# Kernel tuning notes

Hardware: AMD Instinct MI355X
Metric: run time of the kernel (lower is better)

## Reference

```python
import jax, jax.numpy as jnp
import numpy as np

B, GH, GW, DIM, NH = 1, 48, 64, 1536, 16
HD = DIM // NH          # 96
C = HD // 2             # 48, divisible by 3 as the rope split requires
L = max(GH, GW)


def setup_inputs() -> dict:
    key = jax.random.key(0)
    ks = jax.random.split(key, 6)
    x = jax.random.normal(ks[0], (B, GH * GW, DIM), jnp.float32)
    w_init = lambda k: jax.random.normal(k, (DIM, DIM), jnp.float32) * 0.02
    # rope frequency table: theta[p, j] = p / 10000^(j/C); freqs = exp(i*theta)
    pos = jnp.arange(L, dtype=jnp.float32)[:, None]
    inv = 10000.0 ** (-jnp.arange(C, dtype=jnp.float32) / C)
    theta = pos * inv[None, :]
    return {
        "x": x,
        "wq": w_init(ks[1]), "bq": jnp.zeros((DIM,), jnp.float32),
        "wk": w_init(ks[2]), "bk": jnp.zeros((DIM,), jnp.float32),
        "wv": w_init(ks[3]), "bv": jnp.zeros((DIM,), jnp.float32),
        "wo": w_init(ks[4]), "bo": jnp.zeros((DIM,), jnp.float32),
        "freqs_cos": jnp.cos(theta), "freqs_sin": jnp.sin(theta),
        "h": GH, "w": GW,
    }


def rope_apply_spatial(x, freqs_cos, freqs_sin, h, w):
    # x: [b, s, n, d] with s == h*w. Complex rotation done in real arithmetic.
    b, s, n, d = x.shape
    c = d // 2
    c3 = c // 3
    # channel groups: [0:c3] identity (ones), [c3:2c3] rotated by h-position,
    # [2c3:3c3] rotated by w-position  (matches freqs.split + cat in torch)
    cos_hw = jnp.concatenate([
        jnp.ones((h, w, c3), x.dtype),
        jnp.broadcast_to(freqs_cos[:h, None, c3:2 * c3], (h, w, c3)),
        jnp.broadcast_to(freqs_cos[None, :w, 2 * c3:3 * c3], (h, w, c3)),
    ], axis=-1).reshape(1, s, 1, c)
    sin_hw = jnp.concatenate([
        jnp.zeros((h, w, c3), x.dtype),
        jnp.broadcast_to(freqs_sin[:h, None, c3:2 * c3], (h, w, c3)),
        jnp.broadcast_to(freqs_sin[None, :w, 2 * c3:3 * c3], (h, w, c3)),
    ], axis=-1).reshape(1, s, 1, c)
    xc = x.reshape(b, s, n, c, 2)
    xr, xi = xc[..., 0], xc[..., 1]
    yr = xr * cos_hw - xi * sin_hw
    yi = xr * sin_hw + xi * cos_hw
    return jnp.stack([yr, yi], axis=-1).reshape(b, s, n, d)


def reference(x, wq, bq, wk, bk, wv, bv, wo, bo, freqs_cos, freqs_sin, h, w):
    b, s, _ = x.shape
    q = (x @ wq + bq).reshape(b, s, NH, HD)
    k = (x @ wk + bk).reshape(b, s, NH, HD)
    v = (x @ wv + bv).reshape(b, s, NH, HD)
    q = rope_apply_spatial(q, freqs_cos, freqs_sin, h, w)
    k = rope_apply_spatial(k, freqs_cos, freqs_sin, h, w)
    scale = 1.0 / jnp.sqrt(jnp.asarray(HD, q.dtype))
    scores = jnp.einsum('bqnd,bknd->bnqk', q, k) * scale  # [b, n, s, s]
    attn = jax.nn.softmax(scores, axis=-1)
    out = jnp.einsum('bnqk,bknd->bqnd', attn, v).reshape(b, s, NH * HD)
    return out @ wo + bo
```

## Files before the change

### kernel.cpp

```cpp
#include <hip/hip_runtime.h>
#include <math.h>

#define S_LEN 3072
#define DIM 1536
#define NHEADS 16
#define HDIM 96
#define NPAIR 48

typedef __attribute__((ext_vector_type(8))) _Float16 half8;
typedef __attribute__((ext_vector_type(4))) _Float16 half4v;
typedef __attribute__((ext_vector_type(2))) _Float16 half2v;
typedef __attribute__((ext_vector_type(4))) float f32x4;

__device__ inline void gload16(const void* g, void* l) {
    __builtin_amdgcn_global_load_lds(
        (const __attribute__((address_space(1))) void*)g,
        (__attribute__((address_space(3))) void*)l, 16, 0, 0);
}

__global__ __launch_bounds__(256)
void convert_f32_f16(const float* __restrict__ src, _Float16* __restrict__ dst, int n4)
{
    int i = blockIdx.x * 256 + threadIdx.x;
    if (i < n4) {
        float4 v = *(const float4*)&src[(size_t)i * 4];
        half4v h = { (_Float16)v.x, (_Float16)v.y, (_Float16)v.z, (_Float16)v.w };
        *(half4v*)&dst[(size_t)i * 4] = h;
    }
}

__global__ __launch_bounds__(256)
void transpose_w(const float* __restrict__ w0, const float* __restrict__ w1,
                 const float* __restrict__ w2, const float* __restrict__ w3,
                 _Float16* __restrict__ wt)
{
    __shared__ _Float16 t[64][68];
    const int z = blockIdx.z;
    const float* W = (z == 0) ? w0 : (z == 1) ? w1 : (z == 2) ? w2 : w3;
    _Float16* O = wt + (size_t)z * DIM * DIM;
    const int k0 = blockIdx.y * 64, n0 = blockIdx.x * 64;
    const int tid = threadIdx.x;
    const int r = tid >> 4, c4 = (tid & 15) * 4;
#pragma unroll
    for (int g = 0; g < 4; g++) {
        int kk = r + g * 16;
        float4 v = *(const float4*)&W[(size_t)(k0 + kk) * DIM + n0 + c4];
        t[c4 + 0][kk] = (_Float16)v.x; t[c4 + 1][kk] = (_Float16)v.y;
        t[c4 + 2][kk] = (_Float16)v.z; t[c4 + 3][kk] = (_Float16)v.w;
    }
    __syncthreads();
    const int nr = tid >> 2, ks = (tid & 3) * 16;
#pragma unroll
    for (int s = 0; s < 4; s++)
        *(ushort4*)&O[(size_t)(n0 + nr) * DIM + k0 + ks + s * 4] =
            *(ushort4*)&t[nr][ks + s * 4];
}

template<bool QKV>
__global__ __launch_bounds__(256)
void gemm_f16(const _Float16* __restrict__ X,
              const _Float16* __restrict__ W0t, const _Float16* __restrict__ W1t,
              const _Float16* __restrict__ W2t,
              const float* __restrict__ B0, const float* __restrict__ B1,
              const float* __restrict__ B2,
              const float* __restrict__ fc, const float* __restrict__ fs,
              void* __restrict__ outv)
{
    __shared__ __align__(16) _Float16 As[128][64];
    __shared__ __align__(16) _Float16 Bs[128][64];

    const int tid = threadIdx.x;
    const int w = tid >> 6, lane = tid & 63;
    const int ln = lane & 15, quad = lane >> 4;
    const int bz = blockIdx.z;
    const _Float16* Wt = W0t; const float* bias = B0;
    if (QKV) { if (bz == 1) { Wt = W1t; bias = B1; } else if (bz == 2) { Wt = W2t; bias = B2; } }
    const int m0 = blockIdx.y * 128, n0 = blockIdx.x * 128;
    const int wm = w >> 1, wn = w & 1;
    const int row8 = lane >> 3, cch = lane & 7;
    const int gch = cch ^ row8;

    f32x4 acc[4][4];
#pragma unroll
    for (int i = 0; i < 4; i++)
#pragma unroll
        for (int j = 0; j < 4; j++) acc[i][j] = (f32x4){0.f, 0.f, 0.f, 0.f};

    for (int k0 = 0; k0 < DIM; k0 += 64) {
        __syncthreads();
#pragma unroll
        for (int j = 0; j < 4; j++) {
            const int r = w * 32 + j * 8;
            gload16(X  + (size_t)(m0 + r + row8) * DIM + k0 + gch * 8, &As[r][0]);
            gload16(Wt + (size_t)(n0 + r + row8) * DIM + k0 + gch * 8, &Bs[r][0]);
        }
        __syncthreads();

        half8 a[4][2], b[4][2];
#pragma unroll
        for (int mt = 0; mt < 4; mt++) {
            int m = wm * 64 + mt * 16 + ln;
#pragma unroll
            for (int ks = 0; ks < 2; ks++) {
                int s = (ks * 4 + quad) ^ (ln & 7);
                a[mt][ks] = *(const half8*)&As[m][s * 8];
            }
        }
#pragma unroll
        for (int nt = 0; nt < 4; nt++) {
            int n = wn * 64 + nt * 16 + ln;
#pragma unroll
            for (int ks = 0; ks < 2; ks++) {
                int s = (ks * 4 + quad) ^ (ln & 7);
                b[nt][ks] = *(const half8*)&Bs[n][s * 8];
            }
        }
#pragma unroll
        for (int ks = 0; ks < 2; ks++)
#pragma unroll
            for (int mt = 0; mt < 4; mt++)
#pragma unroll
                for (int nt = 0; nt < 4; nt++)
                    acc[mt][nt] = __builtin_amdgcn_mfma_f32_16x16x32_f16(
                        a[mt][ks], b[nt][ks], acc[mt][nt], 0, 0, 0);
    }

#pragma unroll
    for (int nt = 0; nt < 4; nt++) {
        int col = n0 + wn * 64 + nt * 16 + ln;
        float bv = bias[col];
        int head = col / HDIM, hd = col % HDIM;
        int jc = hd >> 1;
        bool isreal = (ln & 1) == 0;
#pragma unroll
        for (int mt = 0; mt < 4; mt++) {
            int row0 = m0 + wm * 64 + mt * 16 + quad * 4;
            if (QKV && bz == 2) {
                half4v p;
#pragma unroll
                for (int r = 0; r < 4; r++) p[r] = (_Float16)(acc[mt][nt][r] + bv);
                *(half4v*)&((_Float16*)outv)[(((size_t)2 * NHEADS + head) * HDIM + hd) * S_LEN + row0] = p;
            } else if (QKV) {
                float v[4], vp[4];
#pragma unroll
                for (int r = 0; r < 4; r++) v[r] = acc[mt][nt][r] + bv;
#pragma unroll
                for (int r = 0; r < 4; r++) vp[r] = __shfl_xor(v[r], 1);
#pragma unroll
                for (int r = 0; r < 4; r++) {
                    int srow = row0 + r;
                    int pos = (jc < 32) ? (srow >> 6) : (srow & 63);
                    float c  = fc[pos * NPAIR + jc];
                    float sn = fs[pos * NPAIR + jc];
                    float xr = isreal ? v[r] : vp[r];
                    float xi = isreal ? vp[r] : v[r];
                    float rot = isreal ? (xr * c - xi * sn) : (xr * sn + xi * c);
                    float outval = (jc < 16) ? v[r] : rot;
                    ((_Float16*)outv)[(((size_t)bz * NHEADS + head) * S_LEN + srow) * HDIM + hd]
                        = (_Float16)outval;
                }
            } else {
#pragma unroll
                for (int r = 0; r < 4; r++)
                    ((float*)outv)[(size_t)(row0 + r) * DIM + col] = acc[mt][nt][r] + bv;
            }
        }
    }
}

__global__ __launch_bounds__(256, 3)
void attn_mfma_kernel(const _Float16* __restrict__ qh, const _Float16* __restrict__ kh,
                      const _Float16* __restrict__ vtg, _Float16* __restrict__ aoh)
{
    __shared__ __align__(16) _Float16 Ks[2][64][104];
    __shared__ __align__(16) _Float16 Vt[2][96][72];

    const int tid  = threadIdx.x;
    const int wid  = tid >> 6;
    const int p    = wid >> 1;
    const int wp   = wid & 1;
    const int lane = tid & 63;
    const int ln   = lane & 15;
    const int quad = lane >> 4;
    const int h    = blockIdx.y;
    const int q0   = blockIdx.x * 64;
    const float scale_ = 0.10206207261596577f * 1.4426950408889634f;
    const int NT = (S_LEN / 2) / 64;

    half8 aq[2][3];
#pragma unroll
    for (int qs = 0; qs < 2; qs++) {
        const _Float16* qrow = qh + (((size_t)h * S_LEN) + q0 + (wp * 2 + qs) * 16 + ln) * HDIM;
#pragma unroll
        for (int kb = 0; kb < 3; kb++) {
            half8 a = *(const half8*)&qrow[kb * 32 + quad * 8];
            half8 v;
#pragma unroll
            for (int i = 0; i < 8; i++) v[i] = (_Float16)((float)a[i] * scale_);
            aq[qs][kb] = v;
        }
    }

    f32x4 o[2][6];
#pragma unroll
    for (int qs = 0; qs < 2; qs++)
#pragma unroll
        for (int dn = 0; dn < 6; dn++) o[qs][dn] = (f32x4){0.f, 0.f, 0.f, 0.f};
    float m_[2] = {-INFINITY, -INFINITY}, l_[2] = {0.f, 0.f};

    const _Float16* kbase = kh + ((size_t)h * S_LEN + p * (S_LEN / 2)) * HDIM;
    const _Float16* vbase = vtg + (size_t)h * HDIM * S_LEN + p * (S_LEN / 2);

    const int tp = tid & 127;
    const int krow = tp >> 1, kc0 = (tp & 1) * 6;
    const _Float16* ksrc0 = kbase + (size_t)krow * HDIM + kc0 * 8;
    _Float16* kdst = &Ks[p][krow][kc0 * 8];
    const int vd0 = tp >> 3, vc = tp & 7;
    const _Float16* vsrc0 = vbase + (size_t)vd0 * S_LEN + vc * 8;
    _Float16* vdst = &Vt[p][vd0][(vc ^ (vd0 & 7)) * 8];

    uint4 kp0, kp1, kp2, kp3, kp4, kp5, vp0, vp1, vp2, vp3, vp4, vp5;
    kp0 = *(const uint4*)(ksrc0 + 0 * 8);  kp1 = *(const uint4*)(ksrc0 + 1 * 8);
    kp2 = *(const uint4*)(ksrc0 + 2 * 8);  kp3 = *(const uint4*)(ksrc0 + 3 * 8);
    kp4 = *(const uint4*)(ksrc0 + 4 * 8);  kp5 = *(const uint4*)(ksrc0 + 5 * 8);
    vp0 = *(const uint4*)(vsrc0 + 0 * 16 * S_LEN);
    vp1 = *(const uint4*)(vsrc0 + 1 * 16 * S_LEN);
    vp2 = *(const uint4*)(vsrc0 + 2 * 16 * S_LEN);
    vp3 = *(const uint4*)(vsrc0 + 3 * 16 * S_LEN);
    vp4 = *(const uint4*)(vsrc0 + 4 * 16 * S_LEN);
    vp5 = *(const uint4*)(vsrc0 + 5 * 16 * S_LEN);

    for (int kt = 0; kt < NT; ++kt) {
        __syncthreads();
        *(uint4*)(kdst + 0 * 8) = kp0;  *(uint4*)(kdst + 1 * 8) = kp1;
        *(uint4*)(kdst + 2 * 8) = kp2;  *(uint4*)(kdst + 3 * 8) = kp3;
        *(uint4*)(kdst + 4 * 8) = kp4;  *(uint4*)(kdst + 5 * 8) = kp5;
        *(uint4*)(vdst + 0 * 16 * 72) = vp0;  *(uint4*)(vdst + 1 * 16 * 72) = vp1;
        *(uint4*)(vdst + 2 * 16 * 72) = vp2;  *(uint4*)(vdst + 3 * 16 * 72) = vp3;
        *(uint4*)(vdst + 4 * 16 * 72) = vp4;  *(uint4*)(vdst + 5 * 16 * 72) = vp5;
        __syncthreads();

        if (kt + 1 < NT) {
            const _Float16* ks2 = ksrc0 + (size_t)(kt + 1) * 64 * HDIM;
            kp0 = *(const uint4*)(ks2 + 0 * 8);  kp1 = *(const uint4*)(ks2 + 1 * 8);
            kp2 = *(const uint4*)(ks2 + 2 * 8);  kp3 = *(const uint4*)(ks2 + 3 * 8);
            kp4 = *(const uint4*)(ks2 + 4 * 8);  kp5 = *(const uint4*)(ks2 + 5 * 8);
            __builtin_amdgcn_sched_barrier(0);
        }

        f32x4 s[2][4];
#pragma unroll
        for (int nb = 0; nb < 4; nb++) {
            half8 ak0 = *(const half8*)&Ks[p][nb * 16 + ln][0 * 32 + quad * 8];
            half8 ak1 = *(const half8*)&Ks[p][nb * 16 + ln][1 * 32 + quad * 8];
            half8 ak2 = *(const half8*)&Ks[p][nb * 16 + ln][2 * 32 + quad * 8];
#pragma unroll
            for (int qs = 0; qs < 2; qs++) {
                f32x4 acc = (f32x4){0.f, 0.f, 0.f, 0.f};
                acc = __builtin_amdgcn_mfma_f32_16x16x32_f16(ak0, aq[qs][0], acc, 0, 0, 0);
                acc = __builtin_amdgcn_mfma_f32_16x16x32_f16(ak1, aq[qs][1], acc, 0, 0, 0);
                acc = __builtin_amdgcn_mfma_f32_16x16x32_f16(ak2, aq[qs][2], acc, 0, 0, 0);
                s[qs][nb] = acc;
            }
        }

        half4v ap[2][4];
#pragma unroll
        for (int qs = 0; qs < 2; qs++) {
            float ma = fmaxf(fmaxf(s[qs][0][0], s[qs][0][1]), fmaxf(s[qs][0][2], s[qs][0][3]));
            float mb = fmaxf(fmaxf(s[qs][1][0], s[qs][1][1]), fmaxf(s[qs][1][2], s[qs][1][3]));
            float mc = fmaxf(fmaxf(s[qs][2][0], s[qs][2][1]), fmaxf(s[qs][2][2], s[qs][2][3]));
            float md = fmaxf(fmaxf(s[qs][3][0], s[qs][3][1]), fmaxf(s[qs][3][2], s[qs][3][3]));
            float mx = fmaxf(fmaxf(ma, mb), fmaxf(mc, md));
            if (!__all(mx <= m_[qs] + 8.0f)) {
                mx = fmaxf(mx, __shfl_xor(mx, 16));
                mx = fmaxf(mx, __shfl_xor(mx, 32));
                float mn = fmaxf(m_[qs], mx);
                float al = __builtin_amdgcn_exp2f(m_[qs] - mn);
                m_[qs] = mn;
                l_[qs] *= al;
#pragma unroll
                for (int dn = 0; dn < 6; dn++)
#pragma unroll
                    for (int r = 0; r < 4; r++) o[qs][dn][r] *= al;
            }
            float rs = 0.f;
            float mq = m_[qs];
#pragma unroll
            for (int nb = 0; nb < 4; nb++) {
                float p0 = __builtin_amdgcn_exp2f(s[qs][nb][0] - mq);
                float p1 = __builtin_amdgcn_exp2f(s[qs][nb][1] - mq);
                float p2 = __builtin_amdgcn_exp2f(s[qs][nb][2] - mq);
                float p3 = __builtin_amdgcn_exp2f(s[qs][nb][3] - mq);
                rs += (p0 + p1) + (p2 + p3);
                half4v pk = { (_Float16)p0, (_Float16)p1, (_Float16)p2, (_Float16)p3 };
                ap[qs][nb] = pk;
            }
            l_[qs] += rs;
        }

        if (kt + 1 < NT) {
            const _Float16* vs2 = vsrc0 + (kt + 1) * 64;
            vp0 = *(const uint4*)(vs2 + 0 * 16 * S_LEN);
            vp1 = *(const uint4*)(vs2 + 1 * 16 * S_LEN);
            vp2 = *(const uint4*)(vs2 + 2 * 16 * S_LEN);
            vp3 = *(const uint4*)(vs2 + 3 * 16 * S_LEN);
            vp4 = *(const uint4*)(vs2 + 4 * 16 * S_LEN);
            vp5 = *(const uint4*)(vs2 + 5 * 16 * S_LEN);
            __builtin_amdgcn_sched_barrier(0);
        }

#pragma unroll
        for (int nb = 0; nb < 4; nb++) {
            const int off = (((nb * 2 + (quad >> 1)) ^ (ln & 7)) * 8) + (quad & 1) * 4;
#pragma unroll
            for (int dn = 0; dn < 6; dn++) {
                half4v av = *(const half4v*)&Vt[p][dn * 16 + ln][off];
                o[0][dn] = __builtin_amdgcn_mfma_f32_16x16x16f16(av, ap[0][nb], o[0][dn], 0, 0, 0);
                o[1][dn] = __builtin_amdgcn_mfma_f32_16x16x16f16(av, ap[1][nb], o[1][dn], 0, 0, 0);
            }
        }
    }

    __syncthreads();
    float lt[2];
#pragma unroll
    for (int qs = 0; qs < 2; qs++) {
        float l = l_[qs];
        l += __shfl_xor(l, 16);
        l += __shfl_xor(l, 32);
        lt[qs] = l;
    }
    float*  scr = (float*)&Ks[0][0][0];
    float2* mlb = (float2*)&Vt[0][0][0];
    if (p == 1) {
#pragma unroll
        for (int qs = 0; qs < 2; qs++) {
            int row = (wp * 2 + qs) * 16 + ln;
            if (quad == 0) mlb[row] = make_float2(m_[qs], lt[qs]);
#pragma unroll
            for (int dn = 0; dn < 6; dn++)
                *(f32x4*)&scr[row * 100 + dn * 16 + quad * 4] = o[qs][dn];
        }
    }
    __syncthreads();
    if (p == 0) {
#pragma unroll
        for (int qs = 0; qs < 2; qs++) {
            int row = (wp * 2 + qs) * 16 + ln;
            float2 ml1 = mlb[row];
            float mm = fmaxf(m_[qs], ml1.x);
            float a0 = __builtin_amdgcn_exp2f(m_[qs] - mm);
            float a1 = __builtin_amdgcn_exp2f(ml1.x - mm);
            float li = 1.0f / (lt[qs] * a0 + ml1.y * a1);
            const size_t rowbase = (size_t)(q0 + row) * DIM + h * HDIM;
#pragma unroll
            for (int dn = 0; dn < 6; dn++) {
                f32x4 o1 = *(const f32x4*)&scr[row * 100 + dn * 16 + quad * 4];
                half4v pk;
#pragma unroll
                for (int r = 0; r < 4; r++)
                    pk[r] = (_Float16)((o[qs][dn][r] * a0 + o1[r] * a1) * li);
                *(half4v*)&aoh[rowbase + dn * 16 + quad * 4] = pk;
            }
        }
    }
}

extern "C" void kernel_launch(void* const* d_in, const int* in_sizes, int n_in,
                              void* d_out, int out_size, void* d_ws, size_t ws_size,
                              hipStream_t stream) {
    const float* x  = (const float*)d_in[0];
    const float* wq = (const float*)d_in[1];
    const float* bq = (const float*)d_in[2];
    const float* wk = (const float*)d_in[3];
    const float* bk = (const float*)d_in[4];
    const float* wv = (const float*)d_in[5];
    const float* bv = (const float*)d_in[6];
    const float* wo = (const float*)d_in[7];
    const float* bo = (const float*)d_in[8];
    const float* fc = (const float*)d_in[9];
    const float* fs = (const float*)d_in[10];
    float* out = (float*)d_out;

    const size_t per  = (size_t)NHEADS * S_LEN * HDIM;
    const size_t dim2 = (size_t)DIM * DIM;
    _Float16* hws  = (_Float16*)d_ws;
    _Float16* qkvh = hws;
    _Float16* qh   = qkvh;
    _Float16* kh   = qkvh + per;
    _Float16* vth  = qkvh + 2 * per;
    _Float16* xh   = hws + 3 * per;
    _Float16* wth  = hws + 4 * per;

    convert_f32_f16<<<(int)((S_LEN * DIM / 4 + 255) / 256), 256, 0, stream>>>(
        x, xh, S_LEN * DIM / 4);
    transpose_w<<<dim3(DIM / 64, DIM / 64, 4), 256, 0, stream>>>(wq, wk, wv, wo, wth);

    gemm_f16<true><<<dim3(DIM / 128, S_LEN / 128, 3), 256, 0, stream>>>(
        xh, wth, wth + dim2, wth + 2 * dim2, bq, bk, bv, fc, fs, qkvh);
    attn_mfma_kernel<<<dim3(S_LEN / 64, NHEADS), 256, 0, stream>>>(qh, kh, vth, xh);
    gemm_f16<false><<<dim3(DIM / 128, S_LEN / 128, 1), 256, 0, stream>>>(
        xh, wth + 3 * dim2, nullptr, nullptr, bo, nullptr, nullptr, fc, fs, out);
}
```

Measured before the change: 331.1 us.

## Double-buffer K via direct global-to-LDS loads; read V straight from global

```diff
diff --git a/kernel.cpp b/kernel.cpp
--- a/kernel.cpp
+++ b/kernel.cpp
@@ -172,8 +172,7 @@
 void attn_mfma_kernel(const _Float16* __restrict__ qh, const _Float16* __restrict__ kh,
                       const _Float16* __restrict__ vtg, _Float16* __restrict__ aoh)
 {
-    __shared__ __align__(16) _Float16 Ks[2][64][104];
-    __shared__ __align__(16) _Float16 Vt[2][96][72];
+    __shared__ __align__(16) _Float16 Kb[2][2][64 * 96];
 
     const int tid  = threadIdx.x;
     const int wid  = tid >> 6;
@@ -208,52 +207,53 @@
         for (int dn = 0; dn < 6; dn++) o[qs][dn] = (f32x4){0.f, 0.f, 0.f, 0.f};
     float m_[2] = {-INFINITY, -INFINITY}, l_[2] = {0.f, 0.f};
 
-    const _Float16* kbase = kh + ((size_t)h * S_LEN + p * (S_LEN / 2)) * HDIM;
-    const _Float16* vbase = vtg + (size_t)h * HDIM * S_LEN + p * (S_LEN / 2);
-
-    const int tp = tid & 127;
-    const int krow = tp >> 1, kc0 = (tp & 1) * 6;
-    const _Float16* ksrc0 = kbase + (size_t)krow * HDIM + kc0 * 8;
-    _Float16* kdst = &Ks[p][krow][kc0 * 8];
-    const int vd0 = tp >> 3, vc = tp & 7;
-    const _Float16* vsrc0 = vbase + (size_t)vd0 * S_LEN + vc * 8;
-    _Float16* vdst = &Vt[p][vd0][(vc ^ (vd0 & 7)) * 8];
-
-    uint4 kp0, kp1, kp2, kp3, kp4, kp5, vp0, vp1, vp2, vp3, vp4, vp5;
-    kp0 = *(const uint4*)(ksrc0 + 0 * 8);  kp1 = *(const uint4*)(ksrc0 + 1 * 8);
-    kp2 = *(const uint4*)(ksrc0 + 2 * 8);  kp3 = *(const uint4*)(ksrc0 + 3 * 8);
-    kp4 = *(const uint4*)(ksrc0 + 4 * 8);  kp5 = *(const uint4*)(ksrc0 + 5 * 8);
-    vp0 = *(const uint4*)(vsrc0 + 0 * 16 * S_LEN);
-    vp1 = *(const uint4*)(vsrc0 + 1 * 16 * S_LEN);
-    vp2 = *(const uint4*)(vsrc0 + 2 * 16 * S_LEN);
-    vp3 = *(const uint4*)(vsrc0 + 3 * 16 * S_LEN);
-    vp4 = *(const uint4*)(vsrc0 + 4 * 16 * S_LEN);
-    vp5 = *(const uint4*)(vsrc0 + 5 * 16 * S_LEN);
+    const char* kbase = (const char*)(kh + ((size_t)h * S_LEN + p * (S_LEN / 2)) * HDIM);
+
+    int koffb[6];
+#pragma unroll
+    for (int i = 0; i < 6; i++) {
+        int pc = i * 128 + (tid & 127);
+        int r  = pc / 12, c = pc - r * 12;
+        int rm = r % 12;
+        int cl = c - rm; if (cl < 0) cl += 12;
+        koffb[i] = r * 192 + cl * 16;
+    }
+    const int A0 = (quad + ln) % 12;
+    int ksel[3];
+    ksel[0] = A0 * 16;
+    { int t1 = A0 + 4; if (t1 >= 12) t1 -= 12; ksel[1] = t1 * 16; }
+    { int t2 = A0 + 8; if (t2 >= 12) t2 -= 12; ksel[2] = t2 * 16; }
+
+    const _Float16* vrow[6];
+#pragma unroll
+    for (int dn = 0; dn < 6; dn++)
+        vrow[dn] = vtg + (size_t)h * HDIM * S_LEN + (size_t)(dn * 16 + ln) * S_LEN
+                 + p * (S_LEN / 2) + quad * 4;
+
+#pragma unroll
+    for (int i = 0; i < 6; i++)
+        gload16(kbase + koffb[i], &Kb[p][0][i * 1024 + wp * 512]);
+    asm volatile("s_waitcnt vmcnt(0)");
+    __syncthreads();
 
     for (int kt = 0; kt < NT; ++kt) {
-        __syncthreads();
-        *(uint4*)(kdst + 0 * 8) = kp0;  *(uint4*)(kdst + 1 * 8) = kp1;
-        *(uint4*)(kdst + 2 * 8) = kp2;  *(uint4*)(kdst + 3 * 8) = kp3;
-        *(uint4*)(kdst + 4 * 8) = kp4;  *(uint4*)(kdst + 5 * 8) = kp5;
-        *(uint4*)(vdst + 0 * 16 * 72) = vp0;  *(uint4*)(vdst + 1 * 16 * 72) = vp1;
-        *(uint4*)(vdst + 2 * 16 * 72) = vp2;  *(uint4*)(vdst + 3 * 16 * 72) = vp3;
-        *(uint4*)(vdst + 4 * 16 * 72) = vp4;  *(uint4*)(vdst + 5 * 16 * 72) = vp5;
-        __syncthreads();
-
+        const int cur = kt & 1;
         if (kt + 1 < NT) {
-            const _Float16* ks2 = ksrc0 + (size_t)(kt + 1) * 64 * HDIM;
-            kp0 = *(const uint4*)(ks2 + 0 * 8);  kp1 = *(const uint4*)(ks2 + 1 * 8);
-            kp2 = *(const uint4*)(ks2 + 2 * 8);  kp3 = *(const uint4*)(ks2 + 3 * 8);
-            kp4 = *(const uint4*)(ks2 + 4 * 8);  kp5 = *(const uint4*)(ks2 + 5 * 8);
+            const char* ks2 = kbase + (size_t)(kt + 1) * 12288;
+#pragma unroll
+            for (int i = 0; i < 6; i++)
+                gload16(ks2 + koffb[i], &Kb[p][cur ^ 1][i * 1024 + wp * 512]);
             __builtin_amdgcn_sched_barrier(0);
         }
 
+        const char* Kc = (const char*)&Kb[p][cur][0];
         f32x4 s[2][4];
 #pragma unroll
         for (int nb = 0; nb < 4; nb++) {
-            half8 ak0 = *(const half8*)&Ks[p][nb * 16 + ln][0 * 32 + quad * 8];
-            half8 ak1 = *(const half8*)&Ks[p][nb * 16 + ln][1 * 32 + quad * 8];
-            half8 ak2 = *(const half8*)&Ks[p][nb * 16 + ln][2 * 32 + quad * 8];
+            const char* krow = Kc + (nb * 16 + ln) * 192;
+            half8 ak0 = *(const half8*)(krow + ksel[(nb + 0) % 3]);
+            half8 ak1 = *(const half8*)(krow + ksel[(nb + 1) % 3]);
+            half8 ak2 = *(const half8*)(krow + ksel[(nb + 2) % 3]);
 #pragma unroll
             for (int qs = 0; qs < 2; qs++) {
                 f32x4 acc = (f32x4){0.f, 0.f, 0.f, 0.f};
@@ -299,30 +299,20 @@
             l_[qs] += rs;
         }
 
-        if (kt + 1 < NT) {
-            const _Float16* vs2 = vsrc0 + (kt + 1) * 64;
-            vp0 = *(const uint4*)(vs2 + 0 * 16 * S_LEN);
-            vp1 = *(const uint4*)(vs2 + 1 * 16 * S_LEN);
-            vp2 = *(const uint4*)(vs2 + 2 * 16 * S_LEN);
-            vp3 = *(const uint4*)(vs2 + 3 * 16 * S_LEN);
-            vp4 = *(const uint4*)(vs2 + 4 * 16 * S_LEN);
-            vp5 = *(const uint4*)(vs2 + 5 * 16 * S_LEN);
-            __builtin_amdgcn_sched_barrier(0);
-        }
-
 #pragma unroll
         for (int nb = 0; nb < 4; nb++) {
-            const int off = (((nb * 2 + (quad >> 1)) ^ (ln & 7)) * 8) + (quad & 1) * 4;
 #pragma unroll
             for (int dn = 0; dn < 6; dn++) {
-                half4v av = *(const half4v*)&Vt[p][dn * 16 + ln][off];
+                half4v av = *(const half4v*)(vrow[dn] + kt * 64 + nb * 16);
                 o[0][dn] = __builtin_amdgcn_mfma_f32_16x16x16f16(av, ap[0][nb], o[0][dn], 0, 0, 0);
                 o[1][dn] = __builtin_amdgcn_mfma_f32_16x16x16f16(av, ap[1][nb], o[1][dn], 0, 0, 0);
             }
         }
-    }
-
-    __syncthreads();
+
+        asm volatile("s_waitcnt vmcnt(0)");
+        __syncthreads();
+    }
+
     float lt[2];
 #pragma unroll
     for (int qs = 0; qs < 2; qs++) {
@@ -331,8 +321,8 @@
         l += __shfl_xor(l, 32);
         lt[qs] = l;
     }
-    float*  scr = (float*)&Ks[0][0][0];
-    float2* mlb = (float2*)&Vt[0][0][0];
+    float*  scr = (float*)&Kb[0][0][0];
+    float2* mlb = (float2*)((char*)&Kb[0][0][0] + 26624);
     if (p == 1) {
 #pragma unroll
         for (int qs = 0; qs < 2; qs++) {
```

After: 442.5 us. 1.34x slower.
